# Kernel optimization log

Hardware: AMD Instinct MI355X
Metric: run time of the kernel (lower is better)

## Reference

```python
import jax, jax.numpy as jnp
import numpy as np

NUM_USERS = 200000
NUM_ITEMS = 100000
EMB_DIM = 64
NUM_EDGES = 3000000


def setup_inputs() -> dict:
    key = jax.random.key(0)
    k1, k2, k3, k4 = jax.random.split(key, 4)
    user_emb = jax.random.normal(k1, (NUM_USERS, EMB_DIM), dtype=jnp.float32)
    item_emb = jax.random.normal(k2, (NUM_ITEMS, EMB_DIM), dtype=jnp.float32)
    src = jax.random.randint(k3, (NUM_EDGES,), 0, NUM_USERS, dtype=jnp.int32)
    dst = jax.random.randint(k4, (NUM_EDGES,), 0, NUM_ITEMS, dtype=jnp.int32)
    return {"user_emb": user_emb, "item_emb": item_emb, "src": src, "dst": dst}


def _mean_agg(x_src, idx_src, idx_dst, n_dst):
    # gather source features along edges, segment-mean into destination nodes
    msg = x_src[idx_src]                                   # [E, D]
    s = jax.ops.segment_sum(msg, idx_dst, num_segments=n_dst)  # [n_dst, D]
    cnt = jax.ops.segment_sum(jnp.ones((idx_dst.shape[0],), x_src.dtype),
                              idx_dst, num_segments=n_dst)      # [n_dst]
    # DGL mean leaves 0 for nodes with no in-edges
    return jnp.where(cnt[:, None] > 0, s / jnp.maximum(cnt, 1)[:, None], 0.0)


def reference(user_emb, item_emb, src, dst):
    n_users = user_emb.shape[0]
    n_items = item_emb.shape[0]

    def layer(u, i):
        # simultaneous bipartite propagation (both use previous-layer inputs)
        i_new = _mean_agg(u, src, dst, n_items)  # items aggregate user neighbors
        u_new = _mean_agg(i, dst, src, n_users)  # users aggregate item neighbors
        return u_new, i_new

    u0, i0 = user_emb, item_emb
    u1, i1 = layer(u0, i0)
    u2, i2 = layer(u1, i1)
    final_user = (u0 + u1 + u2) / 3.0
    final_item = (i0 + i1 + i2) / 3.0
    return final_user, final_item
```

## Files before the change

### kernel.cpp

```cpp
#include <hip/hip_runtime.h>

#define DIM 64
#define NBK 256
#define TEPT 8
#define TSTRIDE 528
#define LDSBUF 14336

typedef unsigned int uint;
typedef unsigned short ushort;

__device__ __forceinline__ float bf16_lo(uint u) {
    union { uint u; float f; } c; c.u = u << 16; return c.f;
}
__device__ __forceinline__ float bf16_hi(uint u) {
    union { uint u; float f; } c; c.u = u & 0xffff0000u; return c.f;
}
__device__ __forceinline__ uint f2b(float f) {
    union { float f; uint u; } c; c.f = f;
    return (c.u + 0x7fffu + ((c.u >> 16) & 1u)) >> 16;
}

__global__ void cvt_bf16_pitch(const float* __restrict__ in, ushort* __restrict__ out,
                               int n8, int pitch, int off) {
    int k = blockIdx.x * blockDim.x + threadIdx.x;
    if (k >= n8) return;
    int row = k >> 3, g = k & 7;
    const float4* p = (const float4*)in + (size_t)k * 2;
    float4 a = p[0], b = p[1];
    uint4 o;
    o.x = f2b(a.x) | (f2b(a.y) << 16);
    o.y = f2b(a.z) | (f2b(a.w) << 16);
    o.z = f2b(b.x) | (f2b(b.y) << 16);
    o.w = f2b(b.z) | (f2b(b.w) << 16);
    *(uint4*)(out + (size_t)row * pitch + off + g * 8) = o;
}

__global__ __launch_bounds__(256) void bin_chunked(
        const int* __restrict__ src, const int* __restrict__ dst,
        int* __restrict__ table, uint* __restrict__ bins,
        int E, int n_users, int nu_pb, int ni_pb) {
    __shared__ int cnt[2 * NBK];
    __shared__ int lbase[2 * NBK + 1];
    __shared__ uint ord[4096];
    for (int i = threadIdx.x; i < 2 * NBK; i += 256) cnt[i] = 0;
    __syncthreads();
    int t0 = blockIdx.x * (256 * TEPT) + threadIdx.x;
    uint st[2 * TEPT];
    #pragma unroll
    for (int k = 0; k < TEPT; ++k) {
        int e = t0 + k * 256;
        if (e < E) {
            int s = src[e], t = dst[e];
            int bu = s / nu_pb;
            int bi = t / ni_pb;
            int ou = atomicAdd(&cnt[bu], 1);
            int oi = atomicAdd(&cnt[NBK + bi], 1);
            st[2 * k]     = ((uint)bu << 12) | (uint)ou;
            st[2 * k + 1] = ((uint)(NBK + bi) << 12) | (uint)oi;
        }
    }
    __syncthreads();
    if (threadIdx.x == 0) {
        int run = 0;
        for (int i = 0; i < 2 * NBK; ++i) { lbase[i] = run; run += cnt[i]; }
        lbase[2 * NBK] = run;
    }
    __syncthreads();
    int* trow = table + (size_t)blockIdx.x * TSTRIDE;
    for (int i = threadIdx.x; i <= 2 * NBK; i += 256) trow[i] = lbase[i];
    #pragma unroll
    for (int k = 0; k < TEPT; ++k) {
        int e = t0 + k * 256;
        if (e < E) {
            int s = src[e], t = dst[e];
            uint su = st[2 * k], si = st[2 * k + 1];
            int bu = (int)(su >> 12);
            int bi = (int)(si >> 12);
            uint wu = (uint)(s - bu * nu_pb) | ((uint)t << 10);
            uint wi = (uint)(t - (bi - NBK) * ni_pb) | ((uint)s << 9);
            ord[lbase[bu] + (int)(su & 4095u)] = wu;
            ord[lbase[bi] + (int)(si & 4095u)] = wi;
        }
    }
    __syncthreads();
    int tot = lbase[2 * NBK];
    uint* slab = bins + (size_t)blockIdx.x * 4096;
    for (int j = threadIdx.x; j < tot; j += 256)
        slab[j] = ord[j];
}

__global__ __launch_bounds__(256) void bucket_sums(
        const int* __restrict__ table, int* __restrict__ btot, int ntiles) {
    int b = blockIdx.x;
    int s = 0;
    for (int t = threadIdx.x; t < ntiles; t += 256) {
        const int* row = table + (size_t)t * TSTRIDE + b;
        s += row[1] - row[0];
    }
    #pragma unroll
    for (int m = 1; m < 64; m <<= 1) s += __shfl_xor(s, m, 64);
    __shared__ int ws[4];
    int lane = threadIdx.x & 63, wid = threadIdx.x >> 6;
    if (lane == 0) ws[wid] = s;
    __syncthreads();
    if (threadIdx.x == 0) btot[b] = ws[0] + ws[1] + ws[2] + ws[3];
}

__global__ void scan512(const int* __restrict__ btot, int* __restrict__ bstart,
                        int* __restrict__ deg, int n_nodes, int total) {
    __shared__ int ws[8];
    int lane = threadIdx.x & 63, wid = threadIdx.x >> 6;
    int v = btot[threadIdx.x];
    int incl = v;
    #pragma unroll
    for (int off = 1; off < 64; off <<= 1) {
        int t = __shfl_up(incl, off, 64);
        if (lane >= off) incl += t;
    }
    if (lane == 63) ws[wid] = incl;
    __syncthreads();
    int woff = 0;
    for (int w = 0; w < wid; ++w) woff += ws[w];
    bstart[threadIdx.x] = woff + incl - v;
    if ((int)threadIdx.x == 511) {
        bstart[512] = total;
        deg[n_nodes] = total;
    }
}

__global__ __launch_bounds__(256) void fill_node(
        const uint* __restrict__ bins, const int* __restrict__ table,
        const int* __restrict__ bstart, int* __restrict__ deg,
        int* __restrict__ col,
        int n_users, int n_items, int ntiles, int nu_pb, int ni_pb) {
    __shared__ int cur[800];
    __shared__ int ws[4];
    __shared__ int lbuf[LDSBUF];
    int b = blockIdx.x;
    bool user = b < NBK;
    int bb = user ? b : b - NBK;
    int npb = user ? nu_pb : ni_pb;
    int ncnt = user ? n_users : n_items;
    int node0 = bb * npb;
    int nn = min(npb, ncnt - node0);
    if (nn <= 0) return;
    int idx0 = (user ? 0 : n_users) + node0;
    int colbase = bstart[b];
    int nedge = bstart[b + 1] - colbase;
    uint mask = user ? 1023u : 511u;
    int shift = user ? 10 : 9;

    for (int i = threadIdx.x; i < nn; i += 256) cur[i] = 0;
    __syncthreads();
    for (int t = threadIdx.x; t < ntiles; t += 256) {
        const int* row = table + (size_t)t * TSTRIDE + b;
        int a = row[0], e2 = row[1];
        const uint* slab = bins + (size_t)t * 4096;
        for (int j = a; j < e2; ++j)
            atomicAdd(&cur[(int)(slab[j] & mask)], 1);
    }
    __syncthreads();
    int CH = (nn + 255) >> 8;
    int c0 = threadIdx.x * CH;
    int s = 0;
    for (int i = 0; i < CH; ++i) {
        int idx = c0 + i;
        if (idx < nn) s += cur[idx];
    }
    int lane = threadIdx.x & 63, wid = threadIdx.x >> 6;
    int incl = s;
    #pragma unroll
    for (int off = 1; off < 64; off <<= 1) {
        int t = __shfl_up(incl, off, 64);
        if (lane >= off) incl += t;
    }
    if (lane == 63) ws[wid] = incl;
    __syncthreads();
    int woff = 0;
    for (int w = 0; w < wid; ++w) woff += ws[w];
    int running = woff + incl - s;
    for (int i = 0; i < CH; ++i) {
        int idx = c0 + i;
        if (idx < nn) {
            int c = cur[idx];
            cur[idx] = running;
            deg[idx0 + idx] = colbase + running;
            running += c;
        }
    }
    __syncthreads();
    if (nedge <= LDSBUF) {
        for (int t = threadIdx.x; t < ntiles; t += 256) {
            const int* row = table + (size_t)t * TSTRIDE + b;
            int a = row[0], e2 = row[1];
            const uint* slab = bins + (size_t)t * 4096;
            for (int j = a; j < e2; ++j) {
                uint w = slab[j];
                int p = atomicAdd(&cur[(int)(w & mask)], 1);
                lbuf[p] = (int)(w >> shift);
            }
        }
        __syncthreads();
        for (int j = threadIdx.x; j < nedge; j += 256)
            col[colbase + j] = lbuf[j];
    } else {
        for (int t = threadIdx.x; t < ntiles; t += 256) {
            const int* row = table + (size_t)t * TSTRIDE + b;
            int a = row[0], e2 = row[1];
            const uint* slab = bins + (size_t)t * 4096;
            for (int j = a; j < e2; ++j) {
                uint w = slab[j];
                int p = atomicAdd(&cur[(int)(w & mask)], 1);
                col[colbase + p] = (int)(w >> shift);
            }
        }
    }
}

template <int COMBINE>
__global__ __launch_bounds__(256) void gather128(
        const ushort* __restrict__ feat,
        const int* __restrict__ ends,
        const int* __restrict__ col,
        const float* __restrict__ x0,
        const ushort* x1, int x1_pitch, int x1_off,
        float* outf,
        ushort* outb, int ob_pitch, int ob_off,
        int n) {
    int node = blockIdx.x * 4 + (threadIdx.x >> 6);
    if (node >= n) return;
    int lane = threadIdx.x & 63;
    int r = lane >> 3, c = lane & 7;
    int beg = ends[node - 1];
    int end = ends[node];
    const ushort* fbase = feat + c * 8;

    float acc[8];
    #pragma unroll
    for (int j = 0; j < 8; ++j) acc[j] = 0.0f;

    for (int e = beg; e < end; e += 16) {
        int i0 = e + r, i1 = e + 8 + r;
        bool ok0 = i0 < end, ok1 = i1 < end;
        int nb0 = col[ok0 ? i0 : beg];
        int nb1 = col[ok1 ? i1 : beg];
        uint4 v0 = *(const uint4*)(fbase + (size_t)nb0 * DIM);
        uint4 v1 = *(const uint4*)(fbase + (size_t)nb1 * DIM);
        if (ok0) {
            acc[0] += bf16_lo(v0.x); acc[1] += bf16_hi(v0.x);
            acc[2] += bf16_lo(v0.y); acc[3] += bf16_hi(v0.y);
            acc[4] += bf16_lo(v0.z); acc[5] += bf16_hi(v0.z);
            acc[6] += bf16_lo(v0.w); acc[7] += bf16_hi(v0.w);
        }
        if (ok1) {
            acc[0] += bf16_lo(v1.x); acc[1] += bf16_hi(v1.x);
            acc[2] += bf16_lo(v1.y); acc[3] += bf16_hi(v1.y);
            acc[4] += bf16_lo(v1.z); acc[5] += bf16_hi(v1.z);
            acc[6] += bf16_lo(v1.w); acc[7] += bf16_hi(v1.w);
        }
    }
    #pragma unroll
    for (int m = 8; m < 64; m <<= 1) {
        #pragma unroll
        for (int j = 0; j < 8; ++j) acc[j] += __shfl_xor(acc[j], m, 64);
    }
    if (r == 0) {
        int d = end - beg;
        float inv = (d > 0) ? 1.0f / (float)d : 0.0f;
        if (COMBINE) {
            size_t base = (size_t)node * DIM + c * 8;
            float4 xa = *(const float4*)(x0 + base);
            float4 xb = *(const float4*)(x0 + base + 4);
            uint4  xq = *(const uint4*)(x1 + (size_t)node * x1_pitch + x1_off + c * 8);
            float4 oa, ob;
            oa.x = (xa.x + bf16_lo(xq.x) + acc[0] * inv) * (1.0f / 3.0f);
            oa.y = (xa.y + bf16_hi(xq.x) + acc[1] * inv) * (1.0f / 3.0f);
            oa.z = (xa.z + bf16_lo(xq.y) + acc[2] * inv) * (1.0f / 3.0f);
            oa.w = (xa.w + bf16_hi(xq.y) + acc[3] * inv) * (1.0f / 3.0f);
            ob.x = (xb.x + bf16_lo(xq.z) + acc[4] * inv) * (1.0f / 3.0f);
            ob.y = (xb.y + bf16_hi(xq.z) + acc[5] * inv) * (1.0f / 3.0f);
            ob.z = (xb.z + bf16_lo(xq.w) + acc[6] * inv) * (1.0f / 3.0f);
            ob.w = (xb.w + bf16_hi(xq.w) + acc[7] * inv) * (1.0f / 3.0f);
            *(float4*)(outf + base)     = oa;
            *(float4*)(outf + base + 4) = ob;
        } else {
            uint4 o;
            o.x = f2b(acc[0] * inv) | (f2b(acc[1] * inv) << 16);
            o.y = f2b(acc[2] * inv) | (f2b(acc[3] * inv) << 16);
            o.z = f2b(acc[4] * inv) | (f2b(acc[5] * inv) << 16);
            o.w = f2b(acc[6] * inv) | (f2b(acc[7] * inv) << 16);
            *(uint4*)(outb + (size_t)node * ob_pitch + ob_off + c * 8) = o;
        }
    }
}

__global__ __launch_bounds__(256) void gather256_combine(
        const ushort* __restrict__ feat,
        const int* __restrict__ ends,
        const int* __restrict__ col,
        const float* __restrict__ x0,
        float* __restrict__ outf,
        ushort* __restrict__ outb,
        int n) {
    int node = blockIdx.x * 4 + (threadIdx.x >> 6);
    if (node >= n) return;
    int lane = threadIdx.x & 63;
    int c = lane & 15, r = lane >> 4;
    int beg = ends[node - 1];
    int end = ends[node];
    const ushort* fbase = feat + c * 8;

    float acc[8];
    #pragma unroll
    for (int j = 0; j < 8; ++j) acc[j] = 0.0f;

    for (int e = beg; e < end; e += 8) {
        int i0 = e + r, i1 = e + 4 + r;
        bool ok0 = i0 < end, ok1 = i1 < end;
        int nb0 = col[ok0 ? i0 : beg];
        int nb1 = col[ok1 ? i1 : beg];
        uint4 v0 = *(const uint4*)(fbase + (size_t)nb0 * 128);
        uint4 v1 = *(const uint4*)(fbase + (size_t)nb1 * 128);
        if (ok0) {
            acc[0] += bf16_lo(v0.x); acc[1] += bf16_hi(v0.x);
            acc[2] += bf16_lo(v0.y); acc[3] += bf16_hi(v0.y);
            acc[4] += bf16_lo(v0.z); acc[5] += bf16_hi(v0.z);
            acc[6] += bf16_lo(v0.w); acc[7] += bf16_hi(v0.w);
        }
        if (ok1) {
            acc[0] += bf16_lo(v1.x); acc[1] += bf16_hi(v1.x);
            acc[2] += bf16_lo(v1.y); acc[3] += bf16_hi(v1.y);
            acc[4] += bf16_lo(v1.z); acc[5] += bf16_hi(v1.z);
            acc[6] += bf16_lo(v1.w); acc[7] += bf16_hi(v1.w);
        }
    }
    #pragma unroll
    for (int m = 16; m < 64; m <<= 1) {
        #pragma unroll
        for (int j = 0; j < 8; ++j) acc[j] += __shfl_xor(acc[j], m, 64);
    }
    float b8[8];
    #pragma unroll
    for (int j = 0; j < 8; ++j) b8[j] = __shfl_xor(acc[j], 8, 64);

    if (r == 0 && c < 8) {
        int d = end - beg;
        float inv = (d > 0) ? 1.0f / (float)d : 0.0f;
        size_t base = (size_t)node * DIM + c * 8;
        float4 xa = *(const float4*)(x0 + base);
        float4 xb = *(const float4*)(x0 + base + 4);
        float i1v[8];
        #pragma unroll
        for (int j = 0; j < 8; ++j) i1v[j] = acc[j] * inv;
        float4 oa, ob;
        oa.x = (xa.x + i1v[0] + b8[0] * inv) * (1.0f / 3.0f);
        oa.y = (xa.y + i1v[1] + b8[1] * inv) * (1.0f / 3.0f);
        oa.z = (xa.z + i1v[2] + b8[2] * inv) * (1.0f / 3.0f);
        oa.w = (xa.w + i1v[3] + b8[3] * inv) * (1.0f / 3.0f);
        ob.x = (xb.x + i1v[4] + b8[4] * inv) * (1.0f / 3.0f);
        ob.y = (xb.y + i1v[5] + b8[5] * inv) * (1.0f / 3.0f);
        ob.z = (xb.z + i1v[6] + b8[6] * inv) * (1.0f / 3.0f);
        ob.w = (xb.w + i1v[7] + b8[7] * inv) * (1.0f / 3.0f);
        *(float4*)(outf + base)     = oa;
        *(float4*)(outf + base + 4) = ob;
        uint4 q;
        q.x = f2b(i1v[0]) | (f2b(i1v[1]) << 16);
        q.y = f2b(i1v[2]) | (f2b(i1v[3]) << 16);
        q.z = f2b(i1v[4]) | (f2b(i1v[5]) << 16);
        q.w = f2b(i1v[6]) | (f2b(i1v[7]) << 16);
        *(uint4*)(outb + base) = q;
    }
}

extern "C" void kernel_launch(void* const* d_in, const int* in_sizes, int n_in,
                              void* d_out, int out_size, void* d_ws, size_t ws_size,
                              hipStream_t stream) {
    const float* u0  = (const float*)d_in[0];
    const float* i0  = (const float*)d_in[1];
    const int*   src = (const int*)d_in[2];
    const int*   dst = (const int*)d_in[3];

    const int n_users = in_sizes[0] / DIM;
    const int n_items = in_sizes[1] / DIM;
    const int E       = in_sizes[2];
    const int n_nodes = n_users + n_items;
    const int nu_pb   = (n_users + NBK - 1) / NBK;
    const int ni_pb   = (n_items + NBK - 1) / NBK;

    const size_t u_elems = (size_t)n_users * DIM;
    const size_t i_elems = (size_t)n_items * DIM;

    int* deg    = (int*)d_ws;
    int* btot   = deg + n_nodes + 1;
    int* bstart = btot + 512;
    int* col    = bstart + 516;
    ushort* ib  = (ushort*)(col + 2 * (size_t)E);

    float* out_u = (float*)d_out;
    float* out_i = out_u + u_elems;
    ushort* u01  = (ushort*)d_out;
    int*   table = (int*)d_out;
    uint*  bins  = (uint*)out_i;

    const int BLK = 256;
    const int ntiles = (E + BLK * TEPT - 1) / (BLK * TEPT);

    bin_chunked<<<ntiles, BLK, 0, stream>>>(src, dst, table, bins,
                                            E, n_users, nu_pb, ni_pb);
    bucket_sums<<<2 * NBK, BLK, 0, stream>>>(table, btot, ntiles);
    scan512<<<1, 512, 0, stream>>>(btot, bstart, deg, n_nodes, 2 * E);
    fill_node<<<2 * NBK, BLK, 0, stream>>>(bins, table, bstart, deg, col,
                                           n_users, n_items, ntiles, nu_pb, ni_pb);

    cvt_bf16_pitch<<<(int)((u_elems / 8 + BLK - 1) / BLK), BLK, 0, stream>>>(
        u0, u01, (int)(u_elems / 8), 128, 0);
    cvt_bf16_pitch<<<(int)((i_elems / 8 + BLK - 1) / BLK), BLK, 0, stream>>>(
        i0, ib, (int)(i_elems / 8), 64, 0);

    const int ug = (n_users + 3) / 4;
    const int ig = (n_items + 3) / 4;

    gather128<0><<<ug, BLK, 0, stream>>>(ib, deg + 1, col, nullptr,
                                         nullptr, 0, 0, nullptr,
                                         u01, 128, 64, n_users);

    gather256_combine<<<ig, BLK, 0, stream>>>(u01, deg + n_users + 1, col,
                                              i0, out_i, ib, n_items);

    gather128<1><<<ug, BLK, 0, stream>>>(ib, deg + 1, col, u0,
                                         u01, 128, 64, out_u,
                                         nullptr, 0, 0, n_users);
}
```

Measured before the change: 573.0 us.

## Double bucket count, parallelize per-tile scan, unroll gather loop to four loads

Doubles the number of node buckets from 256 to 512 per side, so the CSR-building fill_node step runs more, smaller blocks with less LDS each. The serial single-thread prefix over bucket counts in bin_chunked becomes a wave-level shuffle scan across 256 threads. The 128-wide gather loop now issues four neighbor row loads per iteration instead of two, to keep more memory requests in flight. In exchange the per-tile table and the scan grow, and the packed bin word's bit layout changes, which must still fit the node index ranges.

```diff
diff --git a/kernel.cpp b/kernel.cpp
--- a/kernel.cpp
+++ b/kernel.cpp
@@ -1,10 +1,10 @@
 #include <hip/hip_runtime.h>
 
 #define DIM 64
-#define NBK 256
+#define NBK 512
 #define TEPT 8
-#define TSTRIDE 528
-#define LDSBUF 14336
+#define TSTRIDE 1040
+#define LDSBUF 7168
 
 typedef unsigned int uint;
 typedef unsigned short ushort;
@@ -41,6 +41,7 @@
         int E, int n_users, int nu_pb, int ni_pb) {
     __shared__ int cnt[2 * NBK];
     __shared__ int lbase[2 * NBK + 1];
+    __shared__ int ws[4];
     __shared__ uint ord[4096];
     for (int i = threadIdx.x; i < 2 * NBK; i += 256) cnt[i] = 0;
     __syncthreads();
@@ -60,10 +61,27 @@
         }
     }
     __syncthreads();
-    if (threadIdx.x == 0) {
-        int run = 0;
-        for (int i = 0; i < 2 * NBK; ++i) { lbase[i] = run; run += cnt[i]; }
-        lbase[2 * NBK] = run;
+    {
+        int c0 = threadIdx.x * 4;
+        int a0 = cnt[c0], a1 = cnt[c0 + 1], a2 = cnt[c0 + 2], a3 = cnt[c0 + 3];
+        int s4 = a0 + a1 + a2 + a3;
+        int lane = threadIdx.x & 63, wid = threadIdx.x >> 6;
+        int incl = s4;
+        #pragma unroll
+        for (int off = 1; off < 64; off <<= 1) {
+            int t = __shfl_up(incl, off, 64);
+            if (lane >= off) incl += t;
+        }
+        if (lane == 63) ws[wid] = incl;
+        __syncthreads();
+        int woff = 0;
+        for (int w = 0; w < wid; ++w) woff += ws[w];
+        int run = woff + incl - s4;
+        lbase[c0] = run; run += a0;
+        lbase[c0 + 1] = run; run += a1;
+        lbase[c0 + 2] = run; run += a2;
+        lbase[c0 + 3] = run; run += a3;
+        if (threadIdx.x == 255) lbase[2 * NBK] = run;
     }
     __syncthreads();
     int* trow = table + (size_t)blockIdx.x * TSTRIDE;
@@ -75,11 +93,11 @@
             int s = src[e], t = dst[e];
             uint su = st[2 * k], si = st[2 * k + 1];
             int bu = (int)(su >> 12);
-            int bi = (int)(si >> 12);
-            uint wu = (uint)(s - bu * nu_pb) | ((uint)t << 10);
-            uint wi = (uint)(t - (bi - NBK) * ni_pb) | ((uint)s << 9);
+            int bi = (int)(si >> 12) - NBK;
+            uint wu = (uint)(s - bu * nu_pb) | ((uint)t << 9);
+            uint wi = (uint)(t - bi * ni_pb) | ((uint)s << 8);
             ord[lbase[bu] + (int)(su & 4095u)] = wu;
-            ord[lbase[bi] + (int)(si & 4095u)] = wi;
+            ord[lbase[NBK + bi] + (int)(si & 4095u)] = wi;
         }
     }
     __syncthreads();
@@ -106,9 +124,9 @@
     if (threadIdx.x == 0) btot[b] = ws[0] + ws[1] + ws[2] + ws[3];
 }
 
-__global__ void scan512(const int* __restrict__ btot, int* __restrict__ bstart,
-                        int* __restrict__ deg, int n_nodes, int total) {
-    __shared__ int ws[8];
+__global__ void scan1024(const int* __restrict__ btot, int* __restrict__ bstart,
+                         int* __restrict__ deg, int n_nodes, int total) {
+    __shared__ int ws[16];
     int lane = threadIdx.x & 63, wid = threadIdx.x >> 6;
     int v = btot[threadIdx.x];
     int incl = v;
@@ -122,8 +140,8 @@
     int woff = 0;
     for (int w = 0; w < wid; ++w) woff += ws[w];
     bstart[threadIdx.x] = woff + incl - v;
-    if ((int)threadIdx.x == 511) {
-        bstart[512] = total;
+    if ((int)threadIdx.x == 1023) {
+        bstart[1024] = total;
         deg[n_nodes] = total;
     }
 }
@@ -133,7 +151,7 @@
         const int* __restrict__ bstart, int* __restrict__ deg,
         int* __restrict__ col,
         int n_users, int n_items, int ntiles, int nu_pb, int ni_pb) {
-    __shared__ int cur[800];
+    __shared__ int cur[400];
     __shared__ int ws[4];
     __shared__ int lbuf[LDSBUF];
     int b = blockIdx.x;
@@ -147,8 +165,8 @@
     int idx0 = (user ? 0 : n_users) + node0;
     int colbase = bstart[b];
     int nedge = bstart[b + 1] - colbase;
-    uint mask = user ? 1023u : 511u;
-    int shift = user ? 10 : 9;
+    uint mask = user ? 511u : 255u;
+    int shift = user ? 9 : 8;
 
     for (int i = threadIdx.x; i < nn; i += 256) cur[i] = 0;
     __syncthreads();
@@ -314,13 +332,17 @@
     #pragma unroll
     for (int j = 0; j < 8; ++j) acc[j] = 0.0f;
 
-    for (int e = beg; e < end; e += 8) {
-        int i0 = e + r, i1 = e + 4 + r;
-        bool ok0 = i0 < end, ok1 = i1 < end;
+    for (int e = beg; e < end; e += 16) {
+        int i0 = e + r, i1 = e + 4 + r, i2 = e + 8 + r, i3 = e + 12 + r;
+        bool ok0 = i0 < end, ok1 = i1 < end, ok2 = i2 < end, ok3 = i3 < end;
         int nb0 = col[ok0 ? i0 : beg];
         int nb1 = col[ok1 ? i1 : beg];
+        int nb2 = col[ok2 ? i2 : beg];
+        int nb3 = col[ok3 ? i3 : beg];
         uint4 v0 = *(const uint4*)(fbase + (size_t)nb0 * 128);
         uint4 v1 = *(const uint4*)(fbase + (size_t)nb1 * 128);
+        uint4 v2 = *(const uint4*)(fbase + (size_t)nb2 * 128);
+        uint4 v3 = *(const uint4*)(fbase + (size_t)nb3 * 128);
         if (ok0) {
             acc[0] += bf16_lo(v0.x); acc[1] += bf16_hi(v0.x);
             acc[2] += bf16_lo(v0.y); acc[3] += bf16_hi(v0.y);
@@ -332,6 +354,18 @@
             acc[2] += bf16_lo(v1.y); acc[3] += bf16_hi(v1.y);
             acc[4] += bf16_lo(v1.z); acc[5] += bf16_hi(v1.z);
             acc[6] += bf16_lo(v1.w); acc[7] += bf16_hi(v1.w);
+        }
+        if (ok2) {
+            acc[0] += bf16_lo(v2.x); acc[1] += bf16_hi(v2.x);
+            acc[2] += bf16_lo(v2.y); acc[3] += bf16_hi(v2.y);
+            acc[4] += bf16_lo(v2.z); acc[5] += bf16_hi(v2.z);
+            acc[6] += bf16_lo(v2.w); acc[7] += bf16_hi(v2.w);
+        }
+        if (ok3) {
+            acc[0] += bf16_lo(v3.x); acc[1] += bf16_hi(v3.x);
+            acc[2] += bf16_lo(v3.y); acc[3] += bf16_hi(v3.y);
+            acc[4] += bf16_lo(v3.z); acc[5] += bf16_hi(v3.z);
+            acc[6] += bf16_lo(v3.w); acc[7] += bf16_hi(v3.w);
         }
     }
     #pragma unroll
@@ -392,8 +426,8 @@
 
     int* deg    = (int*)d_ws;
     int* btot   = deg + n_nodes + 1;
-    int* bstart = btot + 512;
-    int* col    = bstart + 516;
+    int* bstart = btot + 1024;
+    int* col    = bstart + 1028;
     ushort* ib  = (ushort*)(col + 2 * (size_t)E);
 
     float* out_u = (float*)d_out;
@@ -408,7 +442,7 @@
     bin_chunked<<<ntiles, BLK, 0, stream>>>(src, dst, table, bins,
                                             E, n_users, nu_pb, ni_pb);
     bucket_sums<<<2 * NBK, BLK, 0, stream>>>(table, btot, ntiles);
-    scan512<<<1, 512, 0, stream>>>(btot, bstart, deg, n_nodes, 2 * E);
+    scan1024<<<1, 1024, 0, stream>>>(btot, bstart, deg, n_nodes, 2 * E);
     fill_node<<<2 * NBK, BLK, 0, stream>>>(bins, table, bstart, deg, col,
                                            n_users, n_items, ntiles, nu_pb, ni_pb);
 
```

Measured after the change: 577.8 us. Within noise of the previous version (+0.8%).
